# Optimization experiments

Hardware: AMD Instinct MI355X
Metric: run time of the kernel (lower is better)

The kernel has to match this reference:

```python
import jax, jax.numpy as jnp
import numpy as np

B, S, M, KD, VD, QD, H, NQ = 256, 200, 32, 128, 256, 128, 64, 10000
TA, TB, TC = 0.075, 0.088, 1.0  # triangular membership params a, b, c


def setup_inputs() -> dict:
    key = jax.random.key(0)
    ks = jax.random.split(key, 12)
    q_data = jax.random.randint(ks[0], (B, S), 0, NQ + 1)
    # kaiming-normal-ish embedding table; padding_idx=0 row zeroed
    q_embed_weight = jax.random.normal(ks[1], (NQ + 1, QD)) * np.sqrt(2.0 / QD)
    q_embed_weight = q_embed_weight.at[0].set(0.0)
    key_mem = jax.random.normal(ks[2], (M, KD)) * np.sqrt(2.0 / KD)
    value_mem = jax.random.normal(ks[3], (M, VD)) * np.sqrt(2.0 / VD)
    in_dim = VD + QD
    s = 1.0 / np.sqrt(H)
    W_ih = jax.random.uniform(ks[4], (4 * H, in_dim), minval=-s, maxval=s)
    W_hh = jax.random.uniform(ks[5], (4 * H, H), minval=-s, maxval=s)
    b_ih = jax.random.uniform(ks[6], (4 * H,), minval=-s, maxval=s)
    b_hh = jax.random.uniform(ks[7], (4 * H,), minval=-s, maxval=s)
    W_pred = jax.random.normal(ks[8], (1, H)) * np.sqrt(2.0 / H)
    b_pred = jnp.zeros((1,))
    init_h = jax.random.normal(ks[9], (B, H))
    init_c = jax.random.normal(ks[10], (B, H))
    return dict(q_data=q_data, q_embed_weight=q_embed_weight, key_mem=key_mem,
                value_mem=value_mem, W_ih=W_ih, W_hh=W_hh, b_ih=b_ih, b_hh=b_hh,
                W_pred=W_pred, b_pred=b_pred, init_h=init_h, init_c=init_c)


def triangular_layer(cw):
    """cw: [N, M] correlation weights -> [N] unique-row indices.
    Faithful to torch: trit-quantize each weight {0,1,2}, then map each row to its
    index in the (lexicographically sorted) unique-row table, which is exactly what
    the pairwise squared-distance matmul + (dist==0).nonzero() trick computes."""
    w = jnp.minimum((cw - TA) / (TB - TA), (TC - cw) / (TC - TB))
    w = jnp.maximum(w, 0.0)
    iv = jnp.where(w >= 0.6, 2, jnp.where(w >= 0.1, 1, 0)).astype(jnp.int32)  # [N, M]
    # pack 32 trits into two int32 keys (3^16 < 2^31)
    p = jnp.power(3, jnp.arange(16, dtype=jnp.int32))  # [16]
    kh = (iv[:, :16] * p).sum(1)
    kl = (iv[:, 16:] * p).sum(1)
    order = jnp.lexsort((kl, kh))  # primary key kh
    kh_s, kl_s = kh[order], kl[order]
    change = jnp.concatenate([jnp.zeros((1,), jnp.int32),
                              ((kh_s[1:] != kh_s[:-1]) | (kl_s[1:] != kl_s[:-1])).astype(jnp.int32)])
    rank_sorted = jnp.cumsum(change)
    inv = jnp.zeros(cw.shape[0], jnp.int32).at[order].set(rank_sorted)
    return inv


def reference(q_data, q_embed_weight, key_mem, value_mem, W_ih, W_hh, b_ih, b_hh,
              W_pred, b_pred, init_h, init_c):
    q_emb = q_embed_weight[q_data]                                  # [B,S,QD]
    cw = jax.nn.softmax(jnp.einsum('bsd,md->bsm', q_emb, key_mem))  # DKVMN attention
    read = jnp.einsum('bsm,mv->bsv', cw, value_mem)                 # [B,S,VD]
    ids = triangular_layer(cw.reshape(B * S, M))                    # [B*S]
    x = jnp.concatenate([read, q_emb], axis=-1)                     # [B,S,VD+QD]

    def step(carry, xt):
        h, c = carry
        g = xt @ W_ih.T + h @ W_hh.T + b_ih + b_hh
        i, f, gg, o = jnp.split(g, 4, axis=-1)
        c = jax.nn.sigmoid(f) * c + jax.nn.sigmoid(i) * jnp.tanh(gg)
        h = jax.nn.sigmoid(o) * jnp.tanh(c)
        return (h, c), h

    _, hs = jax.lax.scan(step, (init_h, init_c), jnp.swapaxes(x, 0, 1))
    hs = jnp.swapaxes(hs, 0, 1)                                     # [B,S,H]
    pred = jax.nn.sigmoid(hs @ W_pred.T + b_pred)[..., 0]           # [B,S]
    return pred, ids
```

## Files before the change

kernel.cpp:

```cpp
#include <hip/hip_runtime.h>

#define BB 256
#define SS 200
#define MM 32
#define KDIM 128
#define VDIM 256
#define QDIM 128
#define HH 64
#define NROWS 10001
#define NSAMP (BB*SS)
#define INDIM (VDIM+QDIM)
#define DHS 8192
#define DHMASK (DHS-1)
#define XR 16
#define NB_ATTN 2501

typedef unsigned long long u64;
typedef unsigned int u32;
typedef float f16v __attribute__((ext_vector_type(16)));

__device__ __forceinline__ float fexp(float x){ return __builtin_amdgcn_exp2f(x * 1.44269504f); }
__device__ __forceinline__ float fsigm(float x){ return __builtin_amdgcn_rcpf(1.f + fexp(-x)); }
__device__ __forceinline__ float ftanh(float x){ return 1.f - 2.f*__builtin_amdgcn_rcpf(1.f + fexp(2.f*x)); }
__device__ __forceinline__ int clampq(int q){ return q < 0 ? 0 : (q > NROWS-1 ? NROWS-1 : q); }

__device__ __forceinline__ u32 hash64(u64 x){
  x ^= x >> 33; x *= 0xff51afd7ed558ccdULL;
  x ^= x >> 33; x *= 0xc4ceb9fe1a85ec53ULL;
  x ^= x >> 33;
  return (u32)x;
}

__device__ __forceinline__ u64 shflx64(u64 v, int m){
  int lo = __shfl_xor((int)(u32)v, m, 64);
  int hi = __shfl_xor((int)(u32)(v >> 32), m, 64);
  return ((u64)(u32)hi << 32) | (u32)lo;
}

__global__ void k_tr(const float* __restrict__ W_ih, const float* __restrict__ key_mem,
                     float* __restrict__ WQT4, float* __restrict__ KT,
                     float* __restrict__ WVT, u32* __restrict__ present){
  int idx = blockIdx.x*256 + threadIdx.x;
  if (idx < 131072) {
    int dd = idx & 3, j = (idx >> 2) & 255, d4 = idx >> 10;
    WQT4[idx] = W_ih[j*INDIM + VDIM + 4*d4 + dd];
  } else if (idx < 135168) {
    int t = idx - 131072;
    int m = t & 31, d = t >> 5; KT[t] = key_mem[m*KDIM + d];
  } else if (idx < 200704) {
    int t = idx - 135168;
    int j = t & 255, v = t >> 8; WVT[v*256 + j] = W_ih[j*INDIM + v];
  } else {
    int t = idx - 200704;
    if (t < NROWS) present[t] = 0u;
  }
}

__global__ __launch_bounds__(256) void k_front(
    const float* __restrict__ emb, const float* __restrict__ KT,
    const float* __restrict__ val, const float* __restrict__ WVT,
    const int* __restrict__ q_data,
    float* __restrict__ CW, u64* __restrict__ KEYT,
    float* __restrict__ VW, u32* __restrict__ present){
  int bid = blockIdx.x;
  if (bid < NB_ATTN) {
    int w = threadIdx.x >> 6, l = threadIdx.x & 63;
    int n = bid*4 + w;
    __shared__ float se[4][QDIM];
    bool valid = (n < NROWS);
    if (valid) {
      se[w][l]      = emb[n*QDIM + l];
      se[w][l + 64] = emb[n*QDIM + l + 64];
    }
    __syncthreads();
    int m = l & 31;
    float logit = 0.f;
    if (valid && l < 32)
      for (int d = 0; d < KDIM; ++d) logit += se[w][d] * KT[d*32 + m];
    float mx = logit;
    #pragma unroll
    for (int msk = 16; msk >= 1; msk >>= 1) mx = fmaxf(mx, __shfl_xor(mx, msk, 64));
    float e = (l < 32) ? expf(logit - mx) : 0.f;
    float sum = e;
    #pragma unroll
    for (int msk = 16; msk >= 1; msk >>= 1) sum += __shfl_xor(sum, msk, 64);
    float cw = e / sum;
    float wv = fminf((cw - 0.075f)/0.013f, (1.0f - cw)/0.912f);
    wv = fmaxf(wv, 0.f);
    int iv = (wv >= 0.6f) ? 2 : ((wv >= 0.1f) ? 1 : 0);
    int ee = (m < 16) ? m + 16 : m - 16;
    u64 p3 = 1;
    for (int i = 0; i < 31; ++i) if (i < ee) p3 *= 3ULL;
    u64 term = (valid && l < 32) ? (u64)iv * p3 : 0ULL;
    #pragma unroll
    for (int msk = 16; msk >= 1; msk >>= 1) term += shflx64(term, msk);
    if (valid && l < 32) CW[n*256 + m] = cw;
    if (valid && l == 0) KEYT[n] = term;
  } else if (bid < NB_ATTN + MM) {
    int m = bid - NB_ATTN, j = threadIdx.x;
    __shared__ float sval[VDIM];
    sval[j] = val[m*VDIM + j];
    __syncthreads();
    float a0=0.f, a1=0.f, a2=0.f, a3=0.f;
    for (int v = 0; v < VDIM; v += 4) {
      a0 += sval[v+0]*WVT[(v+0)*256 + j];
      a1 += sval[v+1]*WVT[(v+1)*256 + j];
      a2 += sval[v+2]*WVT[(v+2)*256 + j];
      a3 += sval[v+3]*WVT[(v+3)*256 + j];
    }
    VW[m*256 + j] = (a0+a1)+(a2+a3);
  } else {
    int i = (bid - NB_ATTN - MM)*256 + threadIdx.x;
    if (i < NSAMP) present[clampq(q_data[i])] = 1u;
  }
}

__global__ __launch_bounds__(256) void k_xw(
    const float* __restrict__ CW, const float* __restrict__ emb,
    const float* __restrict__ VW, const float* __restrict__ WQT4,
    const float* __restrict__ b_ih, const float* __restrict__ b_hh,
    float* __restrict__ XW4){
  int base = blockIdx.x * XR;
  int j = threadIdx.x;
  __shared__ float scw[XR][32];
  __shared__ __align__(16) float ses[XR][QDIM];
  for (int idx = j; idx < XR*32; idx += 256) {
    int r = idx >> 5, m = idx & 31, n = base + r;
    scw[r][m] = (n < NROWS) ? CW[n*256 + m] : 0.f;
  }
  for (int idx = j; idx < XR*QDIM; idx += 256) {
    int r = idx >> 7, d = idx & 127, n = base + r;
    ses[r][d] = (n < NROWS) ? emb[n*QDIM + d] : 0.f;
  }
  __syncthreads();
  float bias = b_ih[j] + b_hh[j];
  float acc[XR];
  #pragma unroll
  for (int r = 0; r < XR; ++r) acc[r] = bias;
  for (int m = 0; m < MM; ++m) {
    float wv = VW[m*256 + j];
    #pragma unroll
    for (int r = 0; r < XR; ++r) acc[r] += scw[r][m] * wv;
  }
  for (int d4 = 0; d4 < QDIM/4; ++d4) {
    float4 wq = *(const float4*)(WQT4 + d4*1024 + j*4);
    #pragma unroll
    for (int r = 0; r < XR; ++r) {
      float4 ev = *(const float4*)(&ses[r][4*d4]);
      acc[r] += ev.x*wq.x + ev.y*wq.y + ev.z*wq.z + ev.w*wq.w;
    }
  }
  int gate = j >> 6, unit = j & 63;
  #pragma unroll
  for (int r = 0; r < XR; ++r)
    if (base + r < NROWS) XW4[(size_t)(base + r)*256 + 4*unit + gate] = acc[r];
}

__global__ __launch_bounds__(1024) void k_dedup(
    const u32* __restrict__ present, const u64* __restrict__ KEYT,
    u32* __restrict__ g_htab, u32* __restrict__ g_pay,
    u32* __restrict__ counter, u64* __restrict__ uniq){
  __shared__ u32 sh_tab[DHS];
  __shared__ u32 sh_pay[DHS];
  __shared__ u32 sh_cnt;
  int tid = threadIdx.x;
  for (int i = tid; i < DHS; i += 1024) sh_tab[i] = 0u;
  if (tid == 0) sh_cnt = 0u;
  __syncthreads();
  for (int n = tid; n < NROWS; n += 1024) {
    if (present[n] != 1u) continue;
    u64 key = KEYT[n];
    u32 h = hash64(key) & DHMASK;
    while (true) {
      u32 cur = sh_tab[h];
      if (cur != 0u) {
        if (KEYT[cur-1u] == key) break;
        h = (h + 1) & DHMASK; continue;
      }
      u32 prev = atomicCAS(&sh_tab[h], 0u, (u32)(n + 1));
      if (prev == 0u) {
        u32 idx = atomicAdd(&sh_cnt, 1u);
        uniq[idx] = key;
        sh_pay[h] = idx;
        break;
      }
      if (KEYT[prev-1u] == key) break;
      h = (h + 1) & DHMASK;
    }
  }
  __syncthreads();
  for (int i = tid; i < DHS; i += 1024) {
    u32 v = sh_tab[i];
    g_htab[i] = v;
    g_pay[i]  = v ? sh_pay[i] : 0u;
  }
  if (tid == 0) *counter = sh_cnt;
}

__global__ __launch_bounds__(256) void k_rank(const u64* __restrict__ uniq,
                                              const u32* __restrict__ counter,
                                              u32* __restrict__ RANK){
  __shared__ u64 chunk[2048];
  u32 U = *counter;
  int u = blockIdx.x*256 + threadIdx.x;
  u64 mykey = (u < (int)U) ? uniq[u] : 0;
  u32 cnt = 0;
  for (u32 base = 0; base < U; base += 2048) {
    u32 n = (U - base < 2048u) ? (U - base) : 2048u;
    __syncthreads();
    for (u32 t = threadIdx.x; t < n; t += 256) chunk[t] = uniq[base + t];
    __syncthreads();
    if (u < (int)U)
      for (u32 j = 0; j < n; ++j) cnt += (chunk[j] < mykey) ? 1u : 0u;
  }
  if (u < (int)U) RANK[u] = cnt;
}

__global__ void k_qrank(const u32* __restrict__ present, const u64* __restrict__ KEYT,
                        const u32* __restrict__ g_htab, const u32* __restrict__ g_pay,
                        const u32* __restrict__ RANK, u32* __restrict__ RANKQ){
  int n = blockIdx.x*blockDim.x + threadIdx.x;
  if (n >= NROWS || present[n] != 1u) return;
  u64 key = KEYT[n];
  u32 h = hash64(key) & DHMASK;
  while (true) {
    u32 cur = g_htab[h];
    if (cur != 0u && KEYT[cur-1u] == key) { RANKQ[n] = RANK[g_pay[h]]; return; }
    h = (h + 1) & DHMASK;
  }
}

__global__ void k_ids(const int* __restrict__ q_data, const u32* __restrict__ RANKQ,
                      float* __restrict__ out_ids){
  int i = blockIdx.x*blockDim.x + threadIdx.x;
  if (i >= NSAMP) return;
  out_ids[i] = (float)RANKQ[clampq(q_data[i])];
}

#define DOT16(acc, W, H) do { \
  acc += (W)[0]*(H)[0];   acc += (W)[1]*(H)[1];   acc += (W)[2]*(H)[2];   acc += (W)[3]*(H)[3]; \
  acc += (W)[4]*(H)[4];   acc += (W)[5]*(H)[5];   acc += (W)[6]*(H)[6];   acc += (W)[7]*(H)[7]; \
  acc += (W)[8]*(H)[8];   acc += (W)[9]*(H)[9];   acc += (W)[10]*(H)[10]; acc += (W)[11]*(H)[11]; \
  acc += (W)[12]*(H)[12]; acc += (W)[13]*(H)[13]; acc += (W)[14]*(H)[14]; acc += (W)[15]*(H)[15]; \
} while(0)

__global__ __launch_bounds__(128, 1) void k_lstm(
    const int* __restrict__ q_data, const float* __restrict__ XW4,
    const float* __restrict__ W_hh,
    const float* __restrict__ W_pred, const float* __restrict__ b_pred,
    const float* __restrict__ init_h, const float* __restrict__ init_c,
    float* __restrict__ out_pred){
  const int b = blockIdx.x;
  const int t = threadIdx.x;
  const int w = t >> 6, u = t & 63;
  __shared__ __align__(64) float Hbuf[SS][64];
  __shared__ __align__(16) float4 PART[2][2][64];
  __shared__ int   sq[SS];
  __shared__ float swp[HH];

  for (int s = t; s < SS; s += 128) sq[s] = clampq(q_data[b*SS + s]);
  if (t < HH) swp[t] = W_pred[t];

  const float* wb = W_hh + (size_t)u*HH + 32*w;
  f16v Wi0 = *(const f16v*)(wb +     0), Wi1 = *(const f16v*)(wb +     0 + 16);
  f16v Wf0 = *(const f16v*)(wb +  4096), Wf1 = *(const f16v*)(wb +  4096 + 16);
  f16v Wg0 = *(const f16v*)(wb +  8192), Wg1 = *(const f16v*)(wb +  8192 + 16);
  f16v Wo0 = *(const f16v*)(wb + 12288), Wo1 = *(const f16v*)(wb + 12288 + 16);

  f16v H0, H1;
  {
    const f16v* ihv = (const f16v*)(init_h + (size_t)b*HH + 32*w);
    H0 = ihv[0]; H1 = ihv[1];
  }
  float c  = init_c[b*HH + u];
  float bp = b_pred[0];
  __syncthreads();

  float4 xwA = *(const float4*)(XW4 + (size_t)sq[0]*256 + 4*u);
  float4 xwB = *(const float4*)(XW4 + (size_t)sq[1]*256 + 4*u);

  for (int s = 0; s < SS; ++s) {
    int sp = (s + 2 < SS) ? s + 2 : SS - 1;
    float4 xwC = *(const float4*)(XW4 + (size_t)sq[sp]*256 + 4*u);
    float pi0=0.f,pi1=0.f, pf0=0.f,pf1=0.f, pg0=0.f,pg1=0.f, po0=0.f,po1=0.f;
    DOT16(pi0, Wi0, H0); DOT16(pi1, Wi1, H1);
    DOT16(pf0, Wf0, H0); DOT16(pf1, Wf1, H1);
    DOT16(pg0, Wg0, H0); DOT16(pg1, Wg1, H1);
    DOT16(po0, Wo0, H0); DOT16(po1, Wo1, H1);
    int pr = s & 1;
    PART[pr][w][u] = make_float4(pi0+pi1, pf0+pf1, pg0+pg1, po0+po1);
    __syncthreads();
    float4 oth = PART[pr][w^1][u];
    float ai = xwA.x + ((pi0+pi1) + oth.x);
    float af = xwA.y + ((pf0+pf1) + oth.y);
    float ag = xwA.z + ((pg0+pg1) + oth.z);
    float ao = xwA.w + ((po0+po1) + oth.w);
    c = fsigm(af)*c + fsigm(ai)*ftanh(ag);
    float hh = fsigm(ao)*ftanh(c);
    if ((u >> 5) == w) Hbuf[s][u] = hh;
    const f16v* hb = (const f16v*)(&Hbuf[s][32*w]);
    H0 = hb[0]; H1 = hb[1];
    xwA = xwB; xwB = xwC;
  }
  __syncthreads();

  for (int s = t; s < SS; s += 128) {
    float acc = 0.f;
    #pragma unroll 16
    for (int kk = 0; kk < HH; ++kk) {
      int k2 = (kk + t) & 63;
      acc += Hbuf[s][k2] * swp[k2];
    }
    out_pred[b*SS + s] = fsigm(acc + bp);
  }
}

extern "C" void kernel_launch(void* const* d_in, const int* in_sizes, int n_in,
                              void* d_out, int out_size, void* d_ws, size_t ws_size,
                              hipStream_t stream) {
  const int*   q_data  = (const int*)d_in[0];
  const float* emb     = (const float*)d_in[1];
  const float* keym    = (const float*)d_in[2];
  const float* val     = (const float*)d_in[3];
  const float* W_ih    = (const float*)d_in[4];
  const float* W_hh    = (const float*)d_in[5];
  const float* b_ih    = (const float*)d_in[6];
  const float* b_hh    = (const float*)d_in[7];
  const float* W_pred  = (const float*)d_in[8];
  const float* b_pred  = (const float*)d_in[9];
  const float* init_h  = (const float*)d_in[10];
  const float* init_c  = (const float*)d_in[11];

  char* ws = (char*)d_ws;
  float* XW4     = (float*)(ws + 0);
  float* VW      = (float*)(ws + 10241024);
  u64*  KEYT     = (u64*) (ws + 10273792);
  u64*  uniq     = (u64*) (ws + 10353920);
  u32*  RANK     = (u32*) (ws + 10434048);
  u32*  g_htab   = (u32*) (ws + 10474240);
  u32*  g_pay    = (u32*) (ws + 10507008);
  u32*  counter  = (u32*) (ws + 10539776);
  u32*  present  = (u32*) (ws + 10539840);
  u32*  RANKQ    = (u32*) (ws + 10579904);
  float* WQT4    = (float*)(ws + 10619968);
  float* KT      = (float*)(ws + 11144256);
  float* WVT     = (float*)(ws + 11160640);
  float* CW      = XW4;

  float* out_pred = (float*)d_out;
  float* out_ids  = out_pred + NSAMP;

  hipLaunchKernelGGL(k_tr,    dim3(824), dim3(256), 0, stream,
                     W_ih, keym, WQT4, KT, WVT, present);
  hipLaunchKernelGGL(k_front, dim3(NB_ATTN + MM + 200), dim3(256), 0, stream,
                     emb, KT, val, WVT, q_data, CW, KEYT, VW, present);
  hipLaunchKernelGGL(k_dedup, dim3(1), dim3(1024), 0, stream,
                     present, KEYT, g_htab, g_pay, counter, uniq);
  hipLaunchKernelGGL(k_rank,  dim3((NROWS+255)/256), dim3(256), 0, stream, uniq, counter, RANK);
  hipLaunchKernelGGL(k_qrank, dim3((NROWS+255)/256), dim3(256), 0, stream,
                     present, KEYT, g_htab, g_pay, RANK, RANKQ);
  hipLaunchKernelGGL(k_xw,    dim3((NROWS+XR-1)/XR), dim3(256), 0, stream,
                     CW, emb, VW, WQT4, b_ih, b_hh, XW4);
  hipLaunchKernelGGL(k_ids,   dim3((NSAMP+255)/256), dim3(256), 0, stream, q_data, RANKQ, out_ids);
  hipLaunchKernelGGL(k_lstm,  dim3(BB), dim3(128), 0, stream,
                     q_data, XW4, W_hh, W_pred, b_pred, init_h, init_c, out_pred);
}
```

Measured before the change: 244.5 us.

## Split LSTM recurrent dot across four lane groups with wave shuffle reduction

The LSTM recurrence kernel moves from 128 to 256 threads per batch row. Each wave now owns 16 hidden units, and the 64-wide dot product is split four ways across lane groups. The partial sums are combined with xor shuffles instead of LDS partial buffers, and every lane holds only one 16-wide slice of each gate's weights. This halves the serial FMA chain per timestep, in exchange for extra shuffle latency and a block-wide barrier across four waves each step.

```diff
diff --git a/kernel.cpp b/kernel.cpp
--- a/kernel.cpp
+++ b/kernel.cpp
@@ -244,7 +244,7 @@
   acc += (W)[12]*(H)[12]; acc += (W)[13]*(H)[13]; acc += (W)[14]*(H)[14]; acc += (W)[15]*(H)[15]; \
 } while(0)
 
-__global__ __launch_bounds__(128, 1) void k_lstm(
+__global__ __launch_bounds__(256, 1) void k_lstm(
     const int* __restrict__ q_data, const float* __restrict__ XW4,
     const float* __restrict__ W_hh,
     const float* __restrict__ W_pred, const float* __restrict__ b_pred,
@@ -252,26 +252,23 @@
     float* __restrict__ out_pred){
   const int b = blockIdx.x;
   const int t = threadIdx.x;
-  const int w = t >> 6, u = t & 63;
+  const int w = t >> 6, l = t & 63;
+  const int uo = l & 15, k = l >> 4;
+  const int u = 16*w + uo;
   __shared__ __align__(64) float Hbuf[SS][64];
-  __shared__ __align__(16) float4 PART[2][2][64];
   __shared__ int   sq[SS];
   __shared__ float swp[HH];
 
-  for (int s = t; s < SS; s += 128) sq[s] = clampq(q_data[b*SS + s]);
+  for (int s = t; s < SS; s += 256) sq[s] = clampq(q_data[b*SS + s]);
   if (t < HH) swp[t] = W_pred[t];
 
-  const float* wb = W_hh + (size_t)u*HH + 32*w;
-  f16v Wi0 = *(const f16v*)(wb +     0), Wi1 = *(const f16v*)(wb +     0 + 16);
-  f16v Wf0 = *(const f16v*)(wb +  4096), Wf1 = *(const f16v*)(wb +  4096 + 16);
-  f16v Wg0 = *(const f16v*)(wb +  8192), Wg1 = *(const f16v*)(wb +  8192 + 16);
-  f16v Wo0 = *(const f16v*)(wb + 12288), Wo1 = *(const f16v*)(wb + 12288 + 16);
-
-  f16v H0, H1;
-  {
-    const f16v* ihv = (const f16v*)(init_h + (size_t)b*HH + 32*w);
-    H0 = ihv[0]; H1 = ihv[1];
-  }
+  const float* wb = W_hh + (size_t)u*HH + 16*k;
+  f16v Wi = *(const f16v*)(wb +     0);
+  f16v Wf = *(const f16v*)(wb +  4096);
+  f16v Wg = *(const f16v*)(wb +  8192);
+  f16v Wo = *(const f16v*)(wb + 12288);
+
+  f16v H = *(const f16v*)(init_h + (size_t)b*HH + 16*k);
   float c  = init_c[b*HH + u];
   float bp = b_pred[0];
   __syncthreads();
@@ -282,29 +279,26 @@
   for (int s = 0; s < SS; ++s) {
     int sp = (s + 2 < SS) ? s + 2 : SS - 1;
     float4 xwC = *(const float4*)(XW4 + (size_t)sq[sp]*256 + 4*u);
-    float pi0=0.f,pi1=0.f, pf0=0.f,pf1=0.f, pg0=0.f,pg1=0.f, po0=0.f,po1=0.f;
-    DOT16(pi0, Wi0, H0); DOT16(pi1, Wi1, H1);
-    DOT16(pf0, Wf0, H0); DOT16(pf1, Wf1, H1);
-    DOT16(pg0, Wg0, H0); DOT16(pg1, Wg1, H1);
-    DOT16(po0, Wo0, H0); DOT16(po1, Wo1, H1);
-    int pr = s & 1;
-    PART[pr][w][u] = make_float4(pi0+pi1, pf0+pf1, pg0+pg1, po0+po1);
-    __syncthreads();
-    float4 oth = PART[pr][w^1][u];
-    float ai = xwA.x + ((pi0+pi1) + oth.x);
-    float af = xwA.y + ((pf0+pf1) + oth.y);
-    float ag = xwA.z + ((pg0+pg1) + oth.z);
-    float ao = xwA.w + ((po0+po1) + oth.w);
+    float pi=0.f, pf=0.f, pg=0.f, po=0.f;
+    DOT16(pi, Wi, H); DOT16(pf, Wf, H); DOT16(pg, Wg, H); DOT16(po, Wo, H);
+    pi += __shfl_xor(pi, 16, 64); pf += __shfl_xor(pf, 16, 64);
+    pg += __shfl_xor(pg, 16, 64); po += __shfl_xor(po, 16, 64);
+    pi += __shfl_xor(pi, 32, 64); pf += __shfl_xor(pf, 32, 64);
+    pg += __shfl_xor(pg, 32, 64); po += __shfl_xor(po, 32, 64);
+    float ai = xwA.x + pi;
+    float af = xwA.y + pf;
+    float ag = xwA.z + pg;
+    float ao = xwA.w + po;
     c = fsigm(af)*c + fsigm(ai)*ftanh(ag);
     float hh = fsigm(ao)*ftanh(c);
-    if ((u >> 5) == w) Hbuf[s][u] = hh;
-    const f16v* hb = (const f16v*)(&Hbuf[s][32*w]);
-    H0 = hb[0]; H1 = hb[1];
+    if (l < 16) Hbuf[s][u] = hh;
+    __syncthreads();
+    H = *(const f16v*)(&Hbuf[s][16*k]);
     xwA = xwB; xwB = xwC;
   }
   __syncthreads();
 
-  for (int s = t; s < SS; s += 128) {
+  for (int s = t; s < SS; s += 256) {
     float acc = 0.f;
     #pragma unroll 16
     for (int kk = 0; kk < HH; ++kk) {
@@ -362,6 +356,6 @@
   hipLaunchKernelGGL(k_xw,    dim3((NROWS+XR-1)/XR), dim3(256), 0, stream,
                      CW, emb, VW, WQT4, b_ih, b_hh, XW4);
   hipLaunchKernelGGL(k_ids,   dim3((NSAMP+255)/256), dim3(256), 0, stream, q_data, RANKQ, out_ids);
-  hipLaunchKernelGGL(k_lstm,  dim3(BB), dim3(128), 0, stream,
+  hipLaunchKernelGGL(k_lstm,  dim3(BB), dim3(256), 0, stream,
                      q_data, XW4, W_hh, W_pred, b_pred, init_h, init_c, out_pred);
 }
```

Result: faster. 239.7 us (-2.0%).
